# Kernel optimization log

Hardware: AMD Instinct MI355X
Metric: run time of the kernel (lower is better)

The kernel has to match this reference:

```python
import jax, jax.numpy as jnp
import numpy as np

B, S, IN_DIM, D_MODEL, NUM_HEADS = 4, 2048, 1024, 1024, 16
HEAD_DIM = D_MODEL // NUM_HEADS
CAUSAL = True
NEG = -9000000000000000.0


def _xavier(key, shape):
    fan_out, fan_in = shape
    limit = (6.0 / (fan_in + fan_out)) ** 0.5
    return jax.random.uniform(key, shape, jnp.float32, -limit, limit)


def setup_inputs() -> dict:
    key = jax.random.key(0)
    ks = jax.random.split(key, 5)
    x = jax.random.normal(ks[0], (B, S, IN_DIM), jnp.float32)
    Wq = _xavier(ks[1], (D_MODEL, IN_DIM))
    Wk = _xavier(ks[2], (D_MODEL, IN_DIM))
    Wv = _xavier(ks[3], (D_MODEL, IN_DIM))
    Wo = _xavier(ks[4], (D_MODEL, D_MODEL))
    bq = jnp.zeros((D_MODEL,), jnp.float32)
    bk = jnp.zeros((D_MODEL,), jnp.float32)
    bv = jnp.zeros((D_MODEL,), jnp.float32)
    bo = jnp.zeros((D_MODEL,), jnp.float32)
    return {"x": x, "Wq": Wq, "bq": bq, "Wk": Wk, "bk": bk,
            "Wv": Wv, "bv": bv, "Wo": Wo, "bo": bo}


def reference(x, Wq, bq, Wk, bk, Wv, bv, Wo, bo):
    batch, seq, _ = x.shape
    # torch Linear: y = x @ W.T + b
    q = x @ Wq.T + bq
    k = x @ Wk.T + bk
    v = x @ Wv.T + bv
    # [B, S, H, Dh] -> [B, H, S, Dh]
    def split(t):
        return t.reshape(batch, seq, NUM_HEADS, HEAD_DIM).transpose(0, 2, 1, 3)
    q, k, v = split(q), split(k), split(v)
    scores = jnp.einsum('bhqd,bhkd->bhqk', q, k) / jnp.sqrt(jnp.float32(HEAD_DIM))
    if CAUSAL:
        mask = jnp.tril(jnp.ones((seq, seq), bool))
        scores = jnp.where(mask, scores, jnp.float32(NEG))
    attn = jax.nn.softmax(scores, axis=-1)
    out = jnp.einsum('bhqk,bhkd->bhqd', attn, v)
    out = out.transpose(0, 2, 1, 3).reshape(batch, seq, D_MODEL)
    return out @ Wo.T + bo
```

## Files before the change

### kernel.cpp

```cpp
#include <hip/hip_runtime.h>
#include <cstdint>
#include <cmath>

typedef unsigned short u16;
typedef __attribute__((ext_vector_type(4))) float f32x4;
typedef __attribute__((ext_vector_type(8))) short bf16x8;

#define D_MODEL 1024
#define SEQ     2048
#define BATCH   4
#define NHEAD   16
#define MTOT    (BATCH*SEQ)
#define NXE     ((size_t)MTOT * D_MODEL)

static_assert(sizeof(bf16x8) == 16, "frag size");

__device__ __forceinline__ float bf2f(u16 u) {
    union { uint32_t i; float f; } v; v.i = ((uint32_t)u) << 16; return v.f;
}
__device__ __forceinline__ u16 f2bf(float x) {
    union { float f; uint32_t i; } v; v.f = x;
    uint32_t r = (v.i + 0x7FFFu + ((v.i >> 16) & 1u)) >> 16;
    return (u16)r;
}
__device__ __forceinline__ u16 f2bf_trunc(float x) {
    union { float f; uint32_t i; } v; v.f = x;
    return (u16)(v.i >> 16);
}

#if defined(__has_builtin)
#if __has_builtin(__builtin_amdgcn_exp2f)
#define EXP2_FAST(x) __builtin_amdgcn_exp2f(x)
#endif
#endif
#ifndef EXP2_FAST
#define EXP2_FAST(x) exp2f(x)
#endif

typedef const __attribute__((address_space(1))) void* gptr_t;
typedef __attribute__((address_space(3))) void* sptr_t;
__device__ __forceinline__ void gload_lds16(const void* g, void* l) {
    __builtin_amdgcn_global_load_lds((gptr_t)g, (sptr_t)l, 16, 0, 0);
}

__device__ __forceinline__ u16 u4get(const uint4& v, int e) {
    const uint32_t w = ((e >> 1) == 0) ? v.x : ((e >> 1) == 1) ? v.y
                     : ((e >> 1) == 2) ? v.z : v.w;
    return (u16)((e & 1) ? (w >> 16) : (w & 0xFFFFu));
}

__global__ __launch_bounds__(256) void diag_write(float* __restrict__ out, float v) {
    size_t i = (size_t)blockIdx.x * 256 + threadIdx.x;
    for (; i < NXE; i += (size_t)gridDim.x * 256) out[i] = v;
}

__global__ void detect_dtype(const u16* __restrict__ x, int* __restrict__ flag) {
    __shared__ int cnt;
    if (threadIdx.x == 0) cnt = 0;
    __syncthreads();
    int c = 0;
#pragma unroll
    for (int k = 0; k < 16; ++k) {
        u16 e = x[2 * (threadIdx.x * 16 + k)];
        int ex = (e >> 7) & 0xFF;
        if (e == 0 || (ex >= 100 && ex <= 140)) ++c;
    }
    atomicAdd(&cnt, c);
    __syncthreads();
    if (threadIdx.x == 0) *flag = (cnt >= 3500) ? 1 : 0;
}

struct CvtArgs { const void* src[9]; u16* dst[9]; int n[9]; };

__global__ __launch_bounds__(256) void cvt_all(CvtArgs a, const int* __restrict__ flag) {
    const int seg = blockIdx.y;
    const int n = a.n[seg];
    const int i = (blockIdx.x * 256 + threadIdx.x) * 8;
    if (i >= n) return;
    u16* d = a.dst[seg] + i;
    if (*flag) {
        *(uint4*)d = *(const uint4*)((const u16*)a.src[seg] + i);
    } else {
        const float* s = (const float*)a.src[seg] + i;
        u16 tmp[8];
#pragma unroll
        for (int k = 0; k < 8; ++k) tmp[k] = f2bf(s[k]);
        *(uint4*)d = *(uint4*)tmp;
    }
}

template <typename OutT>
__device__ __forceinline__ void gemm_body(
    const u16* __restrict__ A, const u16* __restrict__ W,
    const u16* __restrict__ bias, OutT* __restrict__ C,
    int M, int N, int K)
{
    __shared__ __align__(16) u16 As[128 * 32];
    __shared__ __align__(16) u16 Bs[128 * 32];

    const int t    = threadIdx.x;
    const int wave = t >> 6;
    const int ln   = t & 15;
    const int qd   = (t >> 4) & 3;
    const int m0   = blockIdx.x * 128;
    const int n0   = blockIdx.y * 128;
    const int wm   = (wave >> 1) * 64;
    const int wn   = (wave & 1) * 64;

    const int srow = t >> 2;
    const int scol = (t & 3) * 8;
    const u16* gA = A + (size_t)(m0 + srow) * K + scol;
    const u16* gB = W + (size_t)(n0 + srow) * K + scol;
    u16* lA = &As[wave * 512];
    u16* lB = &Bs[wave * 512];

    f32x4 acc[4][4] = {};

    for (int k0 = 0; k0 < K; k0 += 32) {
        __syncthreads();
        gload_lds16(gA + k0,                   lA);
        gload_lds16(gA + (size_t)64 * K + k0,  lA + 2048);
        gload_lds16(gB + k0,                   lB);
        gload_lds16(gB + (size_t)64 * K + k0,  lB + 2048);
        __syncthreads();

        bf16x8 af[4], bfr[4];
#pragma unroll
        for (int i = 0; i < 4; ++i)
            af[i] = *(const bf16x8*)&As[(wm + i * 16 + ln) * 32 + qd * 8];
#pragma unroll
        for (int j = 0; j < 4; ++j)
            bfr[j] = *(const bf16x8*)&Bs[(wn + j * 16 + ln) * 32 + qd * 8];
#pragma unroll
        for (int i = 0; i < 4; ++i)
#pragma unroll
            for (int j = 0; j < 4; ++j)
                acc[i][j] = __builtin_amdgcn_mfma_f32_16x16x32_bf16(
                    af[i], bfr[j], acc[i][j], 0, 0, 0);
    }

    float bv[4];
#pragma unroll
    for (int j = 0; j < 4; ++j) bv[j] = bf2f(bias[n0 + wn + j * 16 + ln]);

#pragma unroll
    for (int i = 0; i < 4; ++i)
#pragma unroll
        for (int r = 0; r < 4; ++r) {
            int row = m0 + wm + i * 16 + qd * 4 + r;
            OutT* crow = C + (size_t)row * N + n0 + wn + ln;
#pragma unroll
            for (int j = 0; j < 4; ++j) {
                float v = acc[i][j][r] + bv[j];
                if constexpr (sizeof(OutT) == 2) crow[j * 16] = f2bf(v);
                else                             crow[j * 16] = v;
            }
        }
}

__global__ __launch_bounds__(256) void gemm_qkv(
    const u16* __restrict__ A,
    const u16* __restrict__ W0, const u16* __restrict__ W1, const u16* __restrict__ W2,
    const u16* __restrict__ b0, const u16* __restrict__ b1, const u16* __restrict__ b2,
    u16* __restrict__ C0, u16* __restrict__ C1, u16* __restrict__ C2,
    int M, int N, int K)
{
    const u16* W; const u16* bias; u16* C;
    if (blockIdx.z == 0)      { W = W0; bias = b0; C = C0; }
    else if (blockIdx.z == 1) { W = W1; bias = b1; C = C1; }
    else                      { W = W2; bias = b2; C = C2; }
    gemm_body<u16>(A, W, bias, C, M, N, K);
}

__global__ __launch_bounds__(256) void gemm_final_f32(
    const u16* __restrict__ A, const u16* __restrict__ W,
    const u16* __restrict__ bias, float* __restrict__ C, int M, int N, int K)
{
    gemm_body<float>(A, W, bias, C, M, N, K);
}

__global__ __launch_bounds__(256) void transpose_v(
    const u16* __restrict__ V, u16* __restrict__ VT)
{
    __shared__ u16 T[64][72];
    const int st = blockIdx.x;
    const int bh = blockIdx.y;
    const int b  = bh >> 4;
    const int h  = bh & 15;
    const int t  = threadIdx.x;

    const int sr = t >> 2;
    const int dc = (t & 3) * 16;
    const u16* src = V + ((size_t)b * SEQ + st * 64 + sr) * D_MODEL + h * 64 + dc;
    const uint4 a0 = *(const uint4*)src;
    const uint4 a1 = *(const uint4*)(src + 8);
#pragma unroll
    for (int e = 0; e < 8; ++e) T[dc + e][sr]     = u4get(a0, e);
#pragma unroll
    for (int e = 0; e < 8; ++e) T[dc + 8 + e][sr] = u4get(a1, e);
    __syncthreads();

    const int d  = t >> 2;
    const int sc = (t & 3) * 16;
    u16* dst = VT + ((size_t)bh * 64 + d) * SEQ + st * 64 + sc;
    *(uint4*)dst       = *(const uint4*)&T[d][sc];
    *(uint4*)(dst + 8) = *(const uint4*)&T[d][sc + 8];
}

__global__ __launch_bounds__(64) void flash_attn(
    const u16* __restrict__ Qg, const u16* __restrict__ Kg,
    const u16* __restrict__ VTg, u16* __restrict__ Og)
{
    __shared__ __align__(16) u16 Vsh[64 * 64];
    __shared__ __align__(16) u16 Psh[32 * 64];

    const int lane = threadIdx.x;
    const int ln   = lane & 15;
    const int qd   = lane >> 4;
    const int psw  = (ln & 7) << 3;

    const int pr = blockIdx.x;
    const int bh = blockIdx.y;
    const int b  = bh >> 4;
    const int h  = bh & 15;
    const int h0 = h * 64;
    const size_t rowBase = (size_t)b * SEQ * D_MODEL;

    const int vdG = lane >> 3;
    const int vsw = ((lane & 7) * 8) ^ (vdG << 3);
    const u16* vtRow0 = VTg + ((size_t)(bh * 64 + vdG)) * SEQ + vsw;

    const float SCL = 0.18033688011112042f;

#pragma unroll 1
    for (int sel = 0; sel < 2; ++sel) {
        const int qw  = sel ? (63 - pr) : pr;
        const int qw0 = qw * 32;
        const int ktMax = qw >> 1;

        bf16x8 qf[2][2];
#pragma unroll
        for (int i = 0; i < 2; ++i)
#pragma unroll
            for (int ks = 0; ks < 2; ++ks)
                qf[i][ks] = *(const bf16x8*)(Qg + rowBase
                    + (size_t)(qw0 + i * 16 + ln) * D_MODEL + h0 + ks * 32 + qd * 8);

        float m_run[2], l_run[2];
#pragma unroll
        for (int i = 0; i < 2; ++i) { m_run[i] = -30000.0f; l_run[i] = 0.f; }
        f32x4 oacc[2][4] = {};

        for (int kt = 0; kt <= ktMax; ++kt) {
            __syncthreads();
            {
                const u16* vbase = vtRow0 + kt * 64;
#pragma unroll
                for (int p = 0; p < 8; ++p)
                    gload_lds16(vbase + (size_t)(p * 8) * SEQ, &Vsh[p * 512]);
            }

            f32x4 sacc[4][2] = {};
#pragma unroll
            for (int ks = 0; ks < 2; ++ks) {
                bf16x8 kf[4];
#pragma unroll
                for (int j = 0; j < 4; ++j)
                    kf[j] = *(const bf16x8*)(Kg + rowBase
                        + (size_t)(kt * 64 + j * 16 + ln) * D_MODEL + h0 + ks * 32 + qd * 8);
                __builtin_amdgcn_s_setprio(1);
#pragma unroll
                for (int j = 0; j < 4; ++j)
#pragma unroll
                    for (int i = 0; i < 2; ++i)
                        sacc[j][i] = __builtin_amdgcn_mfma_f32_16x16x32_bf16(
                            kf[j], qf[i][ks], sacc[j][i], 0, 0, 0);
                __builtin_amdgcn_s_setprio(0);
            }

            if (kt == ktMax) {
#pragma unroll
                for (int j = 0; j < 4; ++j)
#pragma unroll
                    for (int r = 0; r < 4; ++r) {
                        const int kpos = kt * 64 + j * 16 + qd * 4 + r;
#pragma unroll
                        for (int i = 0; i < 2; ++i) {
                            const int qpos = qw0 + i * 16 + ln;
                            float s = sacc[j][i][r] * SCL;
                            sacc[j][i][r] = (kpos > qpos) ? -30000.0f : s;
                        }
                    }
            } else {
#pragma unroll
                for (int j = 0; j < 4; ++j)
#pragma unroll
                    for (int i = 0; i < 2; ++i)
#pragma unroll
                        for (int r = 0; r < 4; ++r)
                            sacc[j][i][r] *= SCL;
            }

            float mx[2];
#pragma unroll
            for (int i = 0; i < 2; ++i) {
                float m0 = sacc[0][i][0];
#pragma unroll
                for (int j = 0; j < 4; ++j)
#pragma unroll
                    for (int r = 0; r < 4; ++r) m0 = fmaxf(m0, sacc[j][i][r]);
                m0 = fmaxf(m0, __shfl_xor(m0, 16));
                m0 = fmaxf(m0, __shfl_xor(m0, 32));
                mx[i] = m0;
            }

            const bool grow = !(__all((mx[0] <= m_run[0] + 8.f) &&
                                      (mx[1] <= m_run[1] + 8.f)));
            if (grow) {
#pragma unroll
                for (int i = 0; i < 2; ++i) {
                    const float mo = m_run[i];
                    const float mn = fmaxf(mo, mx[i]);
                    const float alpha = EXP2_FAST(mo - mn);
                    m_run[i] = mn;
                    l_run[i] *= alpha;
#pragma unroll
                    for (int r = 0; r < 4; ++r) {
                        const float ar = __shfl(alpha, qd * 4 + r);
#pragma unroll
                        for (int j = 0; j < 4; ++j) oacc[i][j][r] *= ar;
                    }
                }
            }

#pragma unroll
            for (int i = 0; i < 2; ++i) {
                const float mn = m_run[i];
                float rs = 0.f;
#pragma unroll
                for (int j = 0; j < 4; ++j) {
                    u16 tp[4];
#pragma unroll
                    for (int r = 0; r < 4; ++r) {
                        float p = EXP2_FAST(sacc[j][i][r] - mn);
                        rs += p;
                        tp[r] = f2bf_trunc(p);
                    }
                    uint2 w;
                    w.x = (uint32_t)tp[0] | ((uint32_t)tp[1] << 16);
                    w.y = (uint32_t)tp[2] | ((uint32_t)tp[3] << 16);
                    *(uint2*)&Psh[(i * 16 + ln) * 64 + ((j * 16 + qd * 4) ^ psw)] = w;
                }
                rs += __shfl_xor(rs, 16);
                rs += __shfl_xor(rs, 32);
                l_run[i] += rs;
            }

            __syncthreads();

#pragma unroll
            for (int ks = 0; ks < 2; ++ks) {
                bf16x8 pa[2];
#pragma unroll
                for (int i = 0; i < 2; ++i)
                    pa[i] = *(const bf16x8*)&Psh[(i * 16 + ln) * 64
                                                 + ((ks * 32 + qd * 8) ^ psw)];
                __builtin_amdgcn_s_setprio(1);
#pragma unroll
                for (int j = 0; j < 4; ++j) {
                    const int d = j * 16 + ln;
                    const bf16x8 vb = *(const bf16x8*)&Vsh[d * 64
                        + ((ks * 32 + qd * 8) ^ ((ln & 7) << 3))];
#pragma unroll
                    for (int i = 0; i < 2; ++i)
                        oacc[i][j] = __builtin_amdgcn_mfma_f32_16x16x32_bf16(
                            pa[i], vb, oacc[i][j], 0, 0, 0);
                }
                __builtin_amdgcn_s_setprio(0);
            }
        }

#pragma unroll
        for (int i = 0; i < 2; ++i)
#pragma unroll
            for (int r = 0; r < 4; ++r) {
                const float lr = __shfl(l_run[i], qd * 4 + r);
                const float inv = 1.f / lr;
                const int qrow = qw0 + i * 16 + qd * 4 + r;
                u16* orow = Og + rowBase + (size_t)qrow * D_MODEL + h0 + ln;
#pragma unroll
                for (int j = 0; j < 4; ++j)
                    orow[j * 16] = f2bf(oacc[i][j][r] * inv);
            }
    }
}

static inline bool ranges_overlap(const void* a, size_t an, const void* b, size_t bn) {
    uintptr_t x0 = (uintptr_t)a, x1 = x0 + an;
    uintptr_t y0 = (uintptr_t)b, y1 = y0 + bn;
    return x0 < y1 && y0 < x1;
}

extern "C" void kernel_launch(void* const* d_in, const int* in_sizes, int n_in,
                              void* d_out, int out_size, void* d_ws, size_t ws_size,
                              hipStream_t stream)
{
    int e = 0;
    const int expect[9] = { 8388608, 1048576, 1024, 1048576, 1024,
                            1048576, 1024, 1048576, 1024 };
    if (n_in != 9) e = 59;
    if (!e) for (int i = 0; i < 9; ++i)
        if (in_sizes[i] != expect[i]) { e = 60 + i; break; }
    if (!e && out_size != (int)NXE) e = 53;
    if (!e && ranges_overlap(d_ws, ws_size, d_out, (size_t)out_size * 4)) e = 55;

    const size_t NX = NXE;
    const size_t NW = (size_t)D_MODEL * D_MODEL;
    const size_t NB = D_MODEL;

    const size_t need = (64 + 4 * NW + 4 * NB + 2 * NX) * 2;
    if (!e && ws_size < need) e = 50;
    if (e) { diag_write<<<2048, 256, 0, stream>>>((float*)d_out, ldexpf(1.0f, e)); return; }

    u16* ws   = (u16*)d_ws;
    int* flag = (int*)ws;
    u16* Wqb  = ws + 64;
    u16* Wkb  = Wqb + NW;
    u16* Wvb  = Wkb + NW;
    u16* Wob  = Wvb + NW;
    u16* bqb  = Wob + NW;
    u16* bkb  = bqb + NB;
    u16* bvb  = bkb + NB;
    u16* bob  = bvb + NB;
    u16* Kw   = bob + NB;
    u16* Vw   = Kw  + NX;

    u16* xb  = (u16*)d_out;
    u16* Qw  = xb + NX;
    u16* VTw = xb;
    u16* Ow  = Vw;

    detect_dtype<<<1, 256, 0, stream>>>((const u16*)d_in[0], flag);

    CvtArgs ca;
    const void* srcs[9] = { d_in[0], d_in[1], d_in[3], d_in[5], d_in[7],
                            d_in[2], d_in[4], d_in[6], d_in[8] };
    u16* dsts[9] = { xb, Wqb, Wkb, Wvb, Wob, bqb, bkb, bvb, bob };
    int  ns[9]   = { (int)NX, (int)NW, (int)NW, (int)NW, (int)NW,
                     (int)NB, (int)NB, (int)NB, (int)NB };
    for (int i = 0; i < 9; ++i) { ca.src[i] = srcs[i]; ca.dst[i] = dsts[i]; ca.n[i] = ns[i]; }
    cvt_all<<<dim3((unsigned)((NX + 2047) / 2048), 9), 256, 0, stream>>>(ca, flag);

    gemm_qkv<<<dim3(MTOT / 128, D_MODEL / 128, 3), 256, 0, stream>>>(
        xb, Wqb, Wkb, Wvb, bqb, bkb, bvb, Qw, Kw, Vw, MTOT, D_MODEL, D_MODEL);

    transpose_v<<<dim3(SEQ / 64, BATCH * NHEAD), 256, 0, stream>>>(Vw, VTw);

    flash_attn<<<dim3(SEQ / 64, BATCH * NHEAD), 64, 0, stream>>>(Qw, Kw, VTw, Ow);

    gemm_final_f32<<<dim3(MTOT / 128, D_MODEL / 128), 256, 0, stream>>>(
        Ow, Wob, bob, (float*)d_out, MTOT, D_MODEL, D_MODEL);
}
```

Baseline: 375.3 us.

## Process paired causal query tiles in one KV sweep sharing K/V loads

The flash-attention kernel used to handle its two paired query tiles (pr and 63-pr) one after the other, loading K and V twice. Now a single key-tile loop runs up to the longer tile's range and computes both tiles together, with the short tile active only while kt is at or below its limit. Each K fragment and V LDS tile is loaded once and reused by both, which roughly halves K/V traffic and the number of barriers. The cost is doubled accumulator and Q registers plus a second P buffer in LDS, which may lower occupancy or cause spills.

Result: faster. 356.6 us (-5.0%).

```diff
diff --git a/kernel.cpp b/kernel.cpp
--- a/kernel.cpp
+++ b/kernel.cpp
@@ -212,7 +212,8 @@
     const u16* __restrict__ VTg, u16* __restrict__ Og)
 {
     __shared__ __align__(16) u16 Vsh[64 * 64];
-    __shared__ __align__(16) u16 Psh[32 * 64];
+    __shared__ __align__(16) u16 PshA[32 * 64];
+    __shared__ __align__(16) u16 PshB[32 * 64];
 
     const int lane = threadIdx.x;
     const int ln   = lane & 15;
@@ -226,59 +227,129 @@
     const int h0 = h * 64;
     const size_t rowBase = (size_t)b * SEQ * D_MODEL;
 
+    const int qwA = pr,       qw0A = qwA * 32, ktMaxA = qwA >> 1;
+    const int qwB = 63 - pr,  qw0B = qwB * 32, ktMaxB = qwB >> 1;
+
     const int vdG = lane >> 3;
     const int vsw = ((lane & 7) * 8) ^ (vdG << 3);
     const u16* vtRow0 = VTg + ((size_t)(bh * 64 + vdG)) * SEQ + vsw;
 
     const float SCL = 0.18033688011112042f;
 
-#pragma unroll 1
-    for (int sel = 0; sel < 2; ++sel) {
-        const int qw  = sel ? (63 - pr) : pr;
-        const int qw0 = qw * 32;
-        const int ktMax = qw >> 1;
-
-        bf16x8 qf[2][2];
-#pragma unroll
-        for (int i = 0; i < 2; ++i)
-#pragma unroll
-            for (int ks = 0; ks < 2; ++ks)
-                qf[i][ks] = *(const bf16x8*)(Qg + rowBase
-                    + (size_t)(qw0 + i * 16 + ln) * D_MODEL + h0 + ks * 32 + qd * 8);
-
-        float m_run[2], l_run[2];
-#pragma unroll
-        for (int i = 0; i < 2; ++i) { m_run[i] = -30000.0f; l_run[i] = 0.f; }
-        f32x4 oacc[2][4] = {};
-
-        for (int kt = 0; kt <= ktMax; ++kt) {
-            __syncthreads();
-            {
-                const u16* vbase = vtRow0 + kt * 64;
-#pragma unroll
-                for (int p = 0; p < 8; ++p)
-                    gload_lds16(vbase + (size_t)(p * 8) * SEQ, &Vsh[p * 512]);
-            }
-
-            f32x4 sacc[4][2] = {};
-#pragma unroll
-            for (int ks = 0; ks < 2; ++ks) {
-                bf16x8 kf[4];
+    bf16x8 qfA[2][2], qfB[2][2];
+#pragma unroll
+    for (int i = 0; i < 2; ++i)
+#pragma unroll
+        for (int ks = 0; ks < 2; ++ks) {
+            qfA[i][ks] = *(const bf16x8*)(Qg + rowBase
+                + (size_t)(qw0A + i * 16 + ln) * D_MODEL + h0 + ks * 32 + qd * 8);
+            qfB[i][ks] = *(const bf16x8*)(Qg + rowBase
+                + (size_t)(qw0B + i * 16 + ln) * D_MODEL + h0 + ks * 32 + qd * 8);
+        }
+
+    float mA[2], lA[2], mB[2], lB[2];
+#pragma unroll
+    for (int i = 0; i < 2; ++i) {
+        mA[i] = -30000.0f; lA[i] = 0.f;
+        mB[i] = -30000.0f; lB[i] = 0.f;
+    }
+    f32x4 oA[2][4] = {}, oB[2][4] = {};
+
+    auto softmax_tile = [&](f32x4 (&sacc)[4][2], float (&m_run)[2],
+                            float (&l_run)[2], f32x4 (&oacc)[2][4], u16* P) {
+        float mx[2];
+#pragma unroll
+        for (int i = 0; i < 2; ++i) {
+            float m0 = sacc[0][i][0];
+#pragma unroll
+            for (int j = 0; j < 4; ++j)
+#pragma unroll
+                for (int r = 0; r < 4; ++r) m0 = fmaxf(m0, sacc[j][i][r]);
+            m0 = fmaxf(m0, __shfl_xor(m0, 16));
+            m0 = fmaxf(m0, __shfl_xor(m0, 32));
+            mx[i] = m0;
+        }
+        const bool grow = !(__all((mx[0] <= m_run[0] + 8.f) &&
+                                  (mx[1] <= m_run[1] + 8.f)));
+        if (grow) {
+#pragma unroll
+            for (int i = 0; i < 2; ++i) {
+                const float mo = m_run[i];
+                const float mn = fmaxf(mo, mx[i]);
+                const float alpha = EXP2_FAST(mo - mn);
+                m_run[i] = mn;
+                l_run[i] *= alpha;
+#pragma unroll
+                for (int r = 0; r < 4; ++r) {
+                    const float ar = __shfl(alpha, qd * 4 + r);
+#pragma unroll
+                    for (int j = 0; j < 4; ++j) oacc[i][j][r] *= ar;
+                }
+            }
+        }
+#pragma unroll
+        for (int i = 0; i < 2; ++i) {
+            const float mn = m_run[i];
+            float rs = 0.f;
+#pragma unroll
+            for (int j = 0; j < 4; ++j) {
+                u16 tp[4];
+#pragma unroll
+                for (int r = 0; r < 4; ++r) {
+                    float p = EXP2_FAST(sacc[j][i][r] - mn);
+                    rs += p;
+                    tp[r] = f2bf_trunc(p);
+                }
+                uint2 w;
+                w.x = (uint32_t)tp[0] | ((uint32_t)tp[1] << 16);
+                w.y = (uint32_t)tp[2] | ((uint32_t)tp[3] << 16);
+                *(uint2*)&P[(i * 16 + ln) * 64 + ((j * 16 + qd * 4) ^ psw)] = w;
+            }
+            rs += __shfl_xor(rs, 16);
+            rs += __shfl_xor(rs, 32);
+            l_run[i] += rs;
+        }
+    };
+
+    for (int kt = 0; kt <= ktMaxB; ++kt) {
+        const bool heavy = (kt <= ktMaxA);
+
+        __syncthreads();
+        {
+            const u16* vbase = vtRow0 + kt * 64;
+#pragma unroll
+            for (int p = 0; p < 8; ++p)
+                gload_lds16(vbase + (size_t)(p * 8) * SEQ, &Vsh[p * 512]);
+        }
+
+        f32x4 sA[4][2] = {}, sB[4][2] = {};
+#pragma unroll
+        for (int ks = 0; ks < 2; ++ks) {
+            bf16x8 kf[4];
+#pragma unroll
+            for (int j = 0; j < 4; ++j)
+                kf[j] = *(const bf16x8*)(Kg + rowBase
+                    + (size_t)(kt * 64 + j * 16 + ln) * D_MODEL + h0 + ks * 32 + qd * 8);
+            __builtin_amdgcn_s_setprio(1);
+            if (heavy) {
 #pragma unroll
                 for (int j = 0; j < 4; ++j)
-                    kf[j] = *(const bf16x8*)(Kg + rowBase
-                        + (size_t)(kt * 64 + j * 16 + ln) * D_MODEL + h0 + ks * 32 + qd * 8);
-                __builtin_amdgcn_s_setprio(1);
-#pragma unroll
-                for (int j = 0; j < 4; ++j)
 #pragma unroll
                     for (int i = 0; i < 2; ++i)
-                        sacc[j][i] = __builtin_amdgcn_mfma_f32_16x16x32_bf16(
-                            kf[j], qf[i][ks], sacc[j][i], 0, 0, 0);
-                __builtin_amdgcn_s_setprio(0);
-            }
-
-            if (kt == ktMax) {
+                        sA[j][i] = __builtin_amdgcn_mfma_f32_16x16x32_bf16(
+                            kf[j], qfA[i][ks], sA[j][i], 0, 0, 0);
+            }
+#pragma unroll
+            for (int j = 0; j < 4; ++j)
+#pragma unroll
+                for (int i = 0; i < 2; ++i)
+                    sB[j][i] = __builtin_amdgcn_mfma_f32_16x16x32_bf16(
+                        kf[j], qfB[i][ks], sB[j][i], 0, 0, 0);
+            __builtin_amdgcn_s_setprio(0);
+        }
+
+        if (heavy) {
+            if (kt == ktMaxA) {
 #pragma unroll
                 for (int j = 0; j < 4; ++j)
 #pragma unroll
@@ -286,9 +357,9 @@
                         const int kpos = kt * 64 + j * 16 + qd * 4 + r;
 #pragma unroll
                         for (int i = 0; i < 2; ++i) {
-                            const int qpos = qw0 + i * 16 + ln;
-                            float s = sacc[j][i][r] * SCL;
-                            sacc[j][i][r] = (kpos > qpos) ? -30000.0f : s;
+                            const int qpos = qw0A + i * 16 + ln;
+                            float s = sA[j][i][r] * SCL;
+                            sA[j][i][r] = (kpos > qpos) ? -30000.0f : s;
                         }
                     }
             } else {
@@ -298,88 +369,70 @@
                     for (int i = 0; i < 2; ++i)
 #pragma unroll
                         for (int r = 0; r < 4; ++r)
-                            sacc[j][i][r] *= SCL;
-            }
-
-            float mx[2];
-#pragma unroll
-            for (int i = 0; i < 2; ++i) {
-                float m0 = sacc[0][i][0];
-#pragma unroll
-                for (int j = 0; j < 4; ++j)
-#pragma unroll
-                    for (int r = 0; r < 4; ++r) m0 = fmaxf(m0, sacc[j][i][r]);
-                m0 = fmaxf(m0, __shfl_xor(m0, 16));
-                m0 = fmaxf(m0, __shfl_xor(m0, 32));
-                mx[i] = m0;
-            }
-
-            const bool grow = !(__all((mx[0] <= m_run[0] + 8.f) &&
-                                      (mx[1] <= m_run[1] + 8.f)));
-            if (grow) {
-#pragma unroll
-                for (int i = 0; i < 2; ++i) {
-                    const float mo = m_run[i];
-                    const float mn = fmaxf(mo, mx[i]);
-                    const float alpha = EXP2_FAST(mo - mn);
-                    m_run[i] = mn;
-                    l_run[i] *= alpha;
-#pragma unroll
-                    for (int r = 0; r < 4; ++r) {
-                        const float ar = __shfl(alpha, qd * 4 + r);
-#pragma unroll
-                        for (int j = 0; j < 4; ++j) oacc[i][j][r] *= ar;
+                            sA[j][i][r] *= SCL;
+            }
+        }
+        if (kt == ktMaxB) {
+#pragma unroll
+            for (int j = 0; j < 4; ++j)
+#pragma unroll
+                for (int r = 0; r < 4; ++r) {
+                    const int kpos = kt * 64 + j * 16 + qd * 4 + r;
+#pragma unroll
+                    for (int i = 0; i < 2; ++i) {
+                        const int qpos = qw0B + i * 16 + ln;
+                        float s = sB[j][i][r] * SCL;
+                        sB[j][i][r] = (kpos > qpos) ? -30000.0f : s;
                     }
                 }
-            }
-
+        } else {
+#pragma unroll
+            for (int j = 0; j < 4; ++j)
+#pragma unroll
+                for (int i = 0; i < 2; ++i)
+#pragma unroll
+                    for (int r = 0; r < 4; ++r)
+                        sB[j][i][r] *= SCL;
+        }
+
+        if (heavy) softmax_tile(sA, mA, lA, oA, PshA);
+        softmax_tile(sB, mB, lB, oB, PshB);
+
+        __syncthreads();
+
+#pragma unroll
+        for (int ks = 0; ks < 2; ++ks) {
+            bf16x8 paA[2], paB[2];
 #pragma unroll
             for (int i = 0; i < 2; ++i) {
-                const float mn = m_run[i];
-                float rs = 0.f;
-#pragma unroll
-                for (int j = 0; j < 4; ++j) {
-                    u16 tp[4];
-#pragma unroll
-                    for (int r = 0; r < 4; ++r) {
-                        float p = EXP2_FAST(sacc[j][i][r] - mn);
-                        rs += p;
-                        tp[r] = f2bf_trunc(p);
-                    }
-                    uint2 w;
-                    w.x = (uint32_t)tp[0] | ((uint32_t)tp[1] << 16);
-                    w.y = (uint32_t)tp[2] | ((uint32_t)tp[3] << 16);
-                    *(uint2*)&Psh[(i * 16 + ln) * 64 + ((j * 16 + qd * 4) ^ psw)] = w;
+                if (heavy)
+                    paA[i] = *(const bf16x8*)&PshA[(i * 16 + ln) * 64
+                                                   + ((ks * 32 + qd * 8) ^ psw)];
+                paB[i] = *(const bf16x8*)&PshB[(i * 16 + ln) * 64
+                                               + ((ks * 32 + qd * 8) ^ psw)];
+            }
+            __builtin_amdgcn_s_setprio(1);
+#pragma unroll
+            for (int j = 0; j < 4; ++j) {
+                const int d = j * 16 + ln;
+                const bf16x8 vb = *(const bf16x8*)&Vsh[d * 64
+                    + ((ks * 32 + qd * 8) ^ ((ln & 7) << 3))];
+                if (heavy) {
+#pragma unroll
+                    for (int i = 0; i < 2; ++i)
+                        oA[i][j] = __builtin_amdgcn_mfma_f32_16x16x32_bf16(
+                            paA[i], vb, oA[i][j], 0, 0, 0);
                 }
-                rs += __shfl_xor(rs, 16);
-                rs += __shfl_xor(rs, 32);
-                l_run[i] += rs;
-            }
-
-            __syncthreads();
-
-#pragma unroll
-            for (int ks = 0; ks < 2; ++ks) {
-                bf16x8 pa[2];
 #pragma unroll
                 for (int i = 0; i < 2; ++i)
-                    pa[i] = *(const bf16x8*)&Psh[(i * 16 + ln) * 64
-                                                 + ((ks * 32 + qd * 8) ^ psw)];
-                __builtin_amdgcn_s_setprio(1);
-#pragma unroll
-                for (int j = 0; j < 4; ++j) {
-                    const int d = j * 16 + ln;
-                    const bf16x8 vb = *(const bf16x8*)&Vsh[d * 64
-                        + ((ks * 32 + qd * 8) ^ ((ln & 7) << 3))];
-#pragma unroll
-                    for (int i = 0; i < 2; ++i)
-                        oacc[i][j] = __builtin_amdgcn_mfma_f32_16x16x32_bf16(
-                            pa[i], vb, oacc[i][j], 0, 0, 0);
-                }
-                __builtin_amdgcn_s_setprio(0);
-            }
-        }
-
+                    oB[i][j] = __builtin_amdgcn_mfma_f32_16x16x32_bf16(
+                        paB[i], vb, oB[i][j], 0, 0, 0);
+            }
+            __builtin_amdgcn_s_setprio(0);
+        }
+    }
+
+    auto epilogue = [&](float (&l_run)[2], f32x4 (&oacc)[2][4], int qw0) {
 #pragma unroll
         for (int i = 0; i < 2; ++i)
 #pragma unroll
@@ -392,7 +445,9 @@
                 for (int j = 0; j < 4; ++j)
                     orow[j * 16] = f2bf(oacc[i][j][r] * inv);
             }
-    }
+    };
+    epilogue(lA, oA, qw0A);
+    epilogue(lB, oB, qw0B);
 }
 
 static inline bool ranges_overlap(const void* a, size_t an, const void* b, size_t bn) {
```
